# Kernel tuning notes

Measured on AMD Instinct MI355X. Metric: run time of the kernel, lower is better.

## Reference

```python
import jax, jax.numpy as jnp
import numpy as np

N_NODES = 50000
N_EDGES = 800000
F_IN = 512
NHID = 256
N_CLASSES = 10
N_GRAPHS = 64


def setup_inputs() -> dict:
    key = jax.random.key(0)
    ks = jax.random.split(key, 8)
    x = jax.random.normal(ks[0], (N_NODES, F_IN), dtype=jnp.float32)
    edge_index = jax.random.randint(ks[1], (2, N_EDGES), 0, N_NODES, dtype=jnp.int32)
    # sorted graph-assignment covering all N_GRAPHS segments (global max pool ids)
    batch = ((jnp.arange(N_NODES) * N_GRAPHS) // N_NODES).astype(jnp.int32)
    s1 = 1.0 / np.sqrt(F_IN)
    s2 = 1.0 / np.sqrt(NHID)
    W1 = jax.random.normal(ks[2], (F_IN, NHID), dtype=jnp.float32) * s1
    W2 = jax.random.normal(ks[3], (NHID, NHID), dtype=jnp.float32) * s2
    W3 = jax.random.normal(ks[4], (NHID, NHID), dtype=jnp.float32) * s2
    Wl = jax.random.normal(ks[5], (NHID, N_CLASSES), dtype=jnp.float32) * s2
    b1 = jnp.zeros((NHID,), jnp.float32)
    b2 = jnp.zeros((NHID,), jnp.float32)
    b3 = jnp.zeros((NHID,), jnp.float32)
    bl = jnp.zeros((N_CLASSES,), jnp.float32)
    return dict(x=x, edge_index=edge_index, batch=batch,
                W1=W1, b1=b1, W2=W2, b2=b2, W3=W3, b3=b3, Wl=Wl, bl=bl)


def reference(x, edge_index, batch, W1, b1, W2, b2, W3, b3, Wl, bl):
    n = x.shape[0]
    loop = jnp.arange(n, dtype=edge_index.dtype)
    src = jnp.concatenate([edge_index[0], loop])  # [E+N]
    dst = jnp.concatenate([edge_index[1], loop])
    # symmetric GCN normalization with self-loops: deg >= 1
    deg = jax.ops.segment_sum(jnp.ones_like(dst, jnp.float32), dst, num_segments=n)
    dinv = jax.lax.rsqrt(deg)
    norm = dinv[src] * dinv[dst]  # [E+N]

    def gcn(h, W, b):
        hw = h @ W                                   # [N, H] dense GEMM
        msg = hw[src] * norm[:, None]                # gather + scale [E+N, H]
        agg = jax.ops.segment_sum(msg, dst, num_segments=n)  # scatter-add
        return agg + b

    h = jax.nn.relu(gcn(x, W1, b1))
    h = jax.nn.relu(gcn(h, W2, b2))
    h = jax.nn.relu(gcn(h, W3, b3))
    g = jax.ops.segment_max(h, batch, num_segments=N_GRAPHS)  # global max pool [G, H]
    return jax.nn.log_softmax(g @ Wl + bl, axis=-1)
```

## Files before the change

kernel.cpp:

```cpp
#include <hip/hip_runtime.h>
#include <hip/hip_bf16.h>
#include <cstdint>
#include <cstddef>

typedef __attribute__((ext_vector_type(8))) short short8;
typedef __attribute__((ext_vector_type(4))) float f32x4;

__device__ __forceinline__ unsigned short f32_to_bf16_rn(float f) {
  unsigned int u = __float_as_uint(f);
  u += 0x7FFFu + ((u >> 16) & 1u);
  return (unsigned short)(u >> 16);
}
__device__ __forceinline__ float bf16_to_f32(unsigned short b) {
  return __uint_as_float(((unsigned int)b) << 16);
}
__device__ __forceinline__ void split_bf(float f, unsigned short& hi, unsigned short& lo) {
  hi = f32_to_bf16_rn(f);
  lo = f32_to_bf16_rn(f - bf16_to_f32(hi));
}
__device__ __forceinline__ float4 bf4_to_f4(ushort4 v) {
  float4 r;
  r.x = bf16_to_f32(v.x); r.y = bf16_to_f32(v.y);
  r.z = bf16_to_f32(v.z); r.w = bf16_to_f32(v.w);
  return r;
}

__device__ __forceinline__ void gload16(const void* g, const void* l) {
  __builtin_amdgcn_global_load_lds(
      (const __attribute__((address_space(1))) unsigned int*)g,
      (__attribute__((address_space(3))) unsigned int*)l, 16, 0, 0);
}

__global__ void k_init(int* cnt, int* cursor, float* g, int M, int GH) {
  int i = blockIdx.x * blockDim.x + threadIdx.x;
  int stride = gridDim.x * blockDim.x;
  for (int x = i; x < M; x += stride) { cnt[x] = 0; cursor[x] = 0; }
  for (int x = i; x < GH; x += stride) g[x] = 0.f;
}

__global__ void k_count(const int* __restrict__ dst, int* __restrict__ cnt, int E) {
  int i = blockIdx.x * blockDim.x + threadIdx.x;
  for (int e = i; e < E; e += gridDim.x * blockDim.x)
    atomicAdd(&cnt[dst[e]], 1);
}

__global__ void k_dinv(const int* __restrict__ cnt, float* __restrict__ dinv, int M) {
  int i = blockIdx.x * blockDim.x + threadIdx.x;
  if (i < M) dinv[i] = rsqrtf((float)(cnt[i] + 1));
}

__global__ void k_scan1(const int* __restrict__ cnt, int* __restrict__ excl,
                        int* __restrict__ bsum, int M) {
  __shared__ int s[256];
  int gid = blockIdx.x * 256 + threadIdx.x;
  int v = (gid < M) ? cnt[gid] : 0;
  s[threadIdx.x] = v;
  __syncthreads();
  for (int off = 1; off < 256; off <<= 1) {
    int t = (threadIdx.x >= off) ? s[threadIdx.x - off] : 0;
    __syncthreads();
    s[threadIdx.x] += t;
    __syncthreads();
  }
  if (gid < M) excl[gid] = s[threadIdx.x] - v;
  if (threadIdx.x == 255) bsum[blockIdx.x] = s[255];
}

__global__ void k_scan2(int* bsum, int nb) {
  __shared__ int s[256];
  int v = (threadIdx.x < nb) ? bsum[threadIdx.x] : 0;
  s[threadIdx.x] = v;
  __syncthreads();
  for (int off = 1; off < 256; off <<= 1) {
    int t = (threadIdx.x >= off) ? s[threadIdx.x - off] : 0;
    __syncthreads();
    s[threadIdx.x] += t;
    __syncthreads();
  }
  if (threadIdx.x < nb) bsum[threadIdx.x] = s[threadIdx.x] - v;
}

__global__ void k_scan3(int* row_ptr, const int* __restrict__ bsum, int M, int E) {
  int gid = blockIdx.x * 256 + threadIdx.x;
  if (gid < M) row_ptr[gid] += bsum[blockIdx.x];
  if (gid == 0) row_ptr[M] = E;
}

__global__ void k_scatter(const int* __restrict__ src, const int* __restrict__ dst,
                          const int* __restrict__ row_ptr, int* __restrict__ cursor,
                          int* __restrict__ eidx, int E) {
  int i = blockIdx.x * blockDim.x + threadIdx.x;
  for (int e = i; e < E; e += gridDim.x * blockDim.x) {
    int d = dst[e];
    int pos = atomicAdd(&cursor[d], 1);
    eidx[row_ptr[d] + pos] = src[e];
  }
}

__global__ void k_wtrans(const float* __restrict__ W, unsigned short* __restrict__ WTh,
                         unsigned short* __restrict__ WTl, int K) {
  int idx = blockIdx.x * 256 + threadIdx.x;
  if (idx >= K * 256) return;
  int n = idx / K, k = idx % K;
  float v = W[(size_t)k * 256 + n];
  unsigned short h, l;
  split_bf(v, h, l);
  WTh[(size_t)n * K + k] = h;
  WTl[(size_t)n * K + k] = l;
}

#define BM 64
#define BN 256
#define BK 32

template <bool AF32>
__global__ __launch_bounds__(256) void k_gemm(
    const float* __restrict__ Af,
    const unsigned short* __restrict__ Ahg, const unsigned short* __restrict__ Alg,
    const unsigned short* __restrict__ WTh, const unsigned short* __restrict__ WTl,
    const float* __restrict__ dinv, unsigned short* __restrict__ out, int M, int K) {
  constexpr int AHB = AF32 ? 8192 : 0;
  constexpr int ALB = AHB + 4096;
  constexpr int BHB = AF32 ? 16384 : 8192;
  constexpr int BLB = BHB + 16384;
  constexpr int LDSZ = BLB + 16384;
  __shared__ __align__(16) char lds[LDSZ];

  const int tid = threadIdx.x;
  const int lane = tid & 63;
  const int wv = tid >> 6;
  const int row0 = blockIdx.x * BM;
  const int ASTEP = AF32 ? BK * 4 : BK * 2;

  const char* gsrc[10];
  unsigned ldsoff[10];
#pragma unroll
  for (int i = 0; i < 10; ++i) {
    int c = wv + 4 * i;
    if (i < 2) {
      ldsoff[i] = (unsigned)(c * 1024);
      if constexpr (AF32) {
        int r = c * 8 + (lane >> 3);
        int sslot = (lane & 7) ^ (r & 7);
        int gr = row0 + r; gr = gr < M ? gr : (M - 1);
        gsrc[i] = (const char*)(Af + (size_t)gr * K + sslot * 4);
      } else {
        int plane = c >> 2;
        int r = (c & 3) * 16 + (lane >> 2);
        int sslot = (lane & 3) ^ ((r >> 1) & 3);
        int gr = row0 + r; gr = gr < M ? gr : (M - 1);
        const unsigned short* base = plane ? Alg : Ahg;
        gsrc[i] = (const char*)(base + (size_t)gr * K + sslot * 8);
      }
    } else {
      int cb = c - 8;
      ldsoff[i] = (unsigned)(BHB + cb * 1024);
      int plane = cb >> 4;
      int col = (cb & 15) * 16 + (lane >> 2);
      int sslot = (lane & 3) ^ ((col >> 1) & 3);
      const unsigned short* base = plane ? WTl : WTh;
      gsrc[i] = (const char*)(base + (size_t)col * K + sslot * 8);
    }
  }

  f32x4 acc[4][4] = {};
  const int fr = lane & 15;
  const int ks = lane >> 4;

  for (int k0 = 0; k0 < K; k0 += BK) {
#pragma unroll
    for (int i = 0; i < 10; ++i) {
      gload16(gsrc[i], lds + ldsoff[i]);
      gsrc[i] += (i < 2) ? ASTEP : (BK * 2);
    }
    __syncthreads();

    if constexpr (AF32) {
      int r = tid >> 2, q = tid & 3, rx = r & 7;
      float4 f0 = *(const float4*)&lds[(size_t)r * 128 + (((2 * q) ^ rx) * 16)];
      float4 f1 = *(const float4*)&lds[(size_t)r * 128 + (((2 * q + 1) ^ rx) * 16)];
      float f[8] = {f0.x, f0.y, f0.z, f0.w, f1.x, f1.y, f1.z, f1.w};
      short8 hv, lv;
#pragma unroll
      for (int j = 0; j < 8; ++j) {
        unsigned short h, l;
        split_bf(f[j], h, l);
        hv[j] = (short)h; lv[j] = (short)l;
      }
      int so = (q ^ ((r >> 1) & 3)) * 16;
      *(short8*)&lds[AHB + r * 64 + so] = hv;
      *(short8*)&lds[ALB + r * 64 + so] = lv;
      __syncthreads();
    }

    short8 ah[4], al[4];
#pragma unroll
    for (int m = 0; m < 4; ++m) {
      int rr = m * 16 + fr;
      int so = (ks ^ ((rr >> 1) & 3)) * 16;
      ah[m] = *(const short8*)&lds[AHB + rr * 64 + so];
      al[m] = *(const short8*)&lds[ALB + rr * 64 + so];
    }
#pragma unroll
    for (int n = 0; n < 4; ++n) {
      int cc = wv * 64 + n * 16 + fr;
      int so = (ks ^ ((cc >> 1) & 3)) * 16;
      short8 bh = *(const short8*)&lds[BHB + cc * 64 + so];
      short8 bl = *(const short8*)&lds[BLB + cc * 64 + so];
#pragma unroll
      for (int m = 0; m < 4; ++m) {
        acc[m][n] = __builtin_amdgcn_mfma_f32_16x16x32_bf16(ah[m], bh, acc[m][n], 0, 0, 0);
        acc[m][n] = __builtin_amdgcn_mfma_f32_16x16x32_bf16(ah[m], bl, acc[m][n], 0, 0, 0);
        acc[m][n] = __builtin_amdgcn_mfma_f32_16x16x32_bf16(al[m], bh, acc[m][n], 0, 0, 0);
      }
    }
    __syncthreads();
  }

  const int rq = (lane >> 4) * 4;
#pragma unroll
  for (int m = 0; m < 4; ++m) {
#pragma unroll
    for (int r = 0; r < 4; ++r) {
      int gr = row0 + m * 16 + rq + r;
      if (gr < M) {
        float s = dinv[gr];
#pragma unroll
        for (int n = 0; n < 4; ++n)
          out[(size_t)gr * BN + wv * 64 + n * 16 + fr] = f32_to_bf16_rn(acc[m][n][r] * s);
      }
    }
  }
}

__global__ __launch_bounds__(64) void k_aggregate(
    const unsigned short* __restrict__ hws, const int* __restrict__ eidx,
    const int* __restrict__ row_ptr, const float* __restrict__ dinv,
    const float* __restrict__ bias, unsigned short* __restrict__ out_hi,
    unsigned short* __restrict__ out_lo, float* __restrict__ out_f32, int M) {
  int i = blockIdx.x;
  if (i >= M) return;
  int t = threadIdx.x;
  float4 acc = bf4_to_f4(*(const ushort4*)(hws + (size_t)i * 256 + t * 4));
  int beg = row_ptr[i], end = row_ptr[i + 1];
  int e = beg;
  for (; e + 4 <= end; e += 4) {
    int s0 = eidx[e + 0], s1 = eidx[e + 1], s2 = eidx[e + 2], s3 = eidx[e + 3];
    ushort4 v0 = *(const ushort4*)(hws + (size_t)s0 * 256 + t * 4);
    ushort4 v1 = *(const ushort4*)(hws + (size_t)s1 * 256 + t * 4);
    ushort4 v2 = *(const ushort4*)(hws + (size_t)s2 * 256 + t * 4);
    ushort4 v3 = *(const ushort4*)(hws + (size_t)s3 * 256 + t * 4);
    float4 f0 = bf4_to_f4(v0), f1 = bf4_to_f4(v1);
    float4 f2 = bf4_to_f4(v2), f3 = bf4_to_f4(v3);
    acc.x += (f0.x + f1.x) + (f2.x + f3.x);
    acc.y += (f0.y + f1.y) + (f2.y + f3.y);
    acc.z += (f0.z + f1.z) + (f2.z + f3.z);
    acc.w += (f0.w + f1.w) + (f2.w + f3.w);
  }
  for (; e < end; ++e) {
    int s = eidx[e];
    float4 v = bf4_to_f4(*(const ushort4*)(hws + (size_t)s * 256 + t * 4));
    acc.x += v.x; acc.y += v.y; acc.z += v.z; acc.w += v.w;
  }
  float d = dinv[i];
  float4 b = *(const float4*)(bias + t * 4);
  float r[4];
  r[0] = fmaxf(fmaf(acc.x, d, b.x), 0.f);
  r[1] = fmaxf(fmaf(acc.y, d, b.y), 0.f);
  r[2] = fmaxf(fmaf(acc.z, d, b.z), 0.f);
  r[3] = fmaxf(fmaf(acc.w, d, b.w), 0.f);
  if (out_f32) {
    float4 o; o.x = r[0]; o.y = r[1]; o.z = r[2]; o.w = r[3];
    *(float4*)(out_f32 + (size_t)i * 256 + t * 4) = o;
  } else {
    ushort4 hv, lv;
    unsigned short h, l;
    split_bf(r[0], h, l); hv.x = h; lv.x = l;
    split_bf(r[1], h, l); hv.y = h; lv.y = l;
    split_bf(r[2], h, l); hv.z = h; lv.z = l;
    split_bf(r[3], h, l); hv.w = h; lv.w = l;
    *(ushort4*)(out_hi + (size_t)i * 256 + t * 4) = hv;
    *(ushort4*)(out_lo + (size_t)i * 256 + t * 4) = lv;
  }
}

__global__ __launch_bounds__(256) void k_pool(const float* __restrict__ h,
                                              const int* __restrict__ batch,
                                              float* __restrict__ g, int M) {
  int node0 = blockIdx.x * 32;
  if (node0 >= M) return;
  int t = threadIdx.x;
  int nEnd = min(node0 + 32, M);
  int cur = batch[node0];
  float acc = 0.f;
  for (int n = node0; n < nEnd; ++n) {
    int b = batch[n];
    if (b != cur) {
      atomicMax((int*)&g[(size_t)cur * 256 + t], __float_as_int(acc));
      acc = 0.f; cur = b;
    }
    acc = fmaxf(acc, h[(size_t)n * 256 + t]);
  }
  atomicMax((int*)&g[(size_t)cur * 256 + t], __float_as_int(acc));
}

__global__ __launch_bounds__(256) void k_classify(const float* __restrict__ g,
                                                  const float* __restrict__ Wl,
                                                  const float* __restrict__ bl,
                                                  float* __restrict__ out) {
  __shared__ float sg[256];
  __shared__ float logits[10];
  int b = blockIdx.x;
  sg[threadIdx.x] = g[(size_t)b * 256 + threadIdx.x];
  __syncthreads();
  if (threadIdx.x < 10) {
    float s = bl[threadIdx.x];
    for (int k = 0; k < 256; ++k) s = fmaf(sg[k], Wl[k * 10 + threadIdx.x], s);
    logits[threadIdx.x] = s;
  }
  __syncthreads();
  if (threadIdx.x == 0) {
    float m = logits[0];
    for (int c = 1; c < 10; c++) m = fmaxf(m, logits[c]);
    float sum = 0.f;
    for (int c = 0; c < 10; c++) sum += expf(logits[c] - m);
    float lse = m + logf(sum);
    for (int c = 0; c < 10; c++) out[b * 10 + c] = logits[c] - lse;
  }
}

static inline size_t align256(size_t x) { return (x + 255) & ~(size_t)255; }

extern "C" void kernel_launch(void* const* d_in, const int* in_sizes, int n_in,
                              void* d_out, int out_size, void* d_ws, size_t ws_size,
                              hipStream_t stream) {
  const float* x   = (const float*)d_in[0];
  const int*   ei  = (const int*)d_in[1];
  const int*   bat = (const int*)d_in[2];
  const float* W1  = (const float*)d_in[3];
  const float* b1  = (const float*)d_in[4];
  const float* W2  = (const float*)d_in[5];
  const float* b2  = (const float*)d_in[6];
  const float* W3  = (const float*)d_in[7];
  const float* b3  = (const float*)d_in[8];
  const float* Wl  = (const float*)d_in[9];
  const float* bl  = (const float*)d_in[10];
  float* out = (float*)d_out;

  const int M = in_sizes[0] / 512;
  const int E = in_sizes[1] / 2;
  const int G = out_size / 10;
  const int K1 = 512, H = 256;

  const int* src = ei;
  const int* dst = ei + E;

  char* p = (char*)d_ws;
  size_t off = 0;
  float* p_dinv = (float*)(p + off); off = align256(off + (size_t)M * 4);
  int* cnt      = (int*)(p + off);   off = align256(off + (size_t)M * 4);
  int* cursor   = (int*)(p + off);   off = align256(off + (size_t)M * 4);
  int* row_ptr  = (int*)(p + off);   off = align256(off + ((size_t)M + 1) * 4);
  int* bsum     = (int*)(p + off);   off = align256(off + 256 * 4);
  int* eidx     = (int*)(p + off);   off = align256(off + (size_t)E * 4);
  float* g      = (float*)(p + off); off = align256(off + (size_t)G * H * 4);
  unsigned short* WT1h = (unsigned short*)(p + off); off = align256(off + (size_t)H * K1 * 2);
  unsigned short* WT1l = (unsigned short*)(p + off); off = align256(off + (size_t)H * K1 * 2);
  unsigned short* WT2h = (unsigned short*)(p + off); off = align256(off + (size_t)H * H * 2);
  unsigned short* WT2l = (unsigned short*)(p + off); off = align256(off + (size_t)H * H * 2);
  unsigned short* WT3h = (unsigned short*)(p + off); off = align256(off + (size_t)H * H * 2);
  unsigned short* WT3l = (unsigned short*)(p + off); off = align256(off + (size_t)H * H * 2);
  unsigned short* hws = (unsigned short*)(p + off); off = align256(off + (size_t)M * H * 2);
  unsigned short* h_hi = (unsigned short*)(p + off); off += (size_t)M * H * 2;
  unsigned short* h_lo = (unsigned short*)(p + off); off = align256(off + (size_t)M * H * 2);
  float* bufC = (float*)h_hi;
  (void)ws_size;

  int nb = (M + 255) / 256;

  k_init<<<256, 256, 0, stream>>>(cnt, cursor, g, M, G * H);
  k_count<<<1024, 256, 0, stream>>>(dst, cnt, E);
  k_dinv<<<nb, 256, 0, stream>>>(cnt, p_dinv, M);
  k_scan1<<<nb, 256, 0, stream>>>(cnt, row_ptr, bsum, M);
  k_scan2<<<1, 256, 0, stream>>>(bsum, nb);
  k_scan3<<<nb, 256, 0, stream>>>(row_ptr, bsum, M, E);
  k_scatter<<<1024, 256, 0, stream>>>(src, dst, row_ptr, cursor, eidx, E);

  k_wtrans<<<(H * K1 + 255) / 256, 256, 0, stream>>>(W1, WT1h, WT1l, K1);
  k_wtrans<<<(H * H + 255) / 256, 256, 0, stream>>>(W2, WT2h, WT2l, H);
  k_wtrans<<<(H * H + 255) / 256, 256, 0, stream>>>(W3, WT3h, WT3l, H);

  int gblk = (M + BM - 1) / BM;
  k_gemm<true><<<gblk, 256, 0, stream>>>(x, nullptr, nullptr, WT1h, WT1l, p_dinv, hws, M, K1);
  k_aggregate<<<M, 64, 0, stream>>>(hws, eidx, row_ptr, p_dinv, b1, h_hi, h_lo, nullptr, M);
  k_gemm<false><<<gblk, 256, 0, stream>>>(nullptr, h_hi, h_lo, WT2h, WT2l, p_dinv, hws, M, H);
  k_aggregate<<<M, 64, 0, stream>>>(hws, eidx, row_ptr, p_dinv, b2, h_hi, h_lo, nullptr, M);
  k_gemm<false><<<gblk, 256, 0, stream>>>(nullptr, h_hi, h_lo, WT3h, WT3l, p_dinv, hws, M, H);
  k_aggregate<<<M, 64, 0, stream>>>(hws, eidx, row_ptr, p_dinv, b3, nullptr, nullptr, bufC, M);

  k_pool<<<(M + 31) / 32, 256, 0, stream>>>(bufC, bat, g, M);
  k_classify<<<G, 256, 0, stream>>>(g, Wl, bl, out);
}
```

Measured before the change: 598.5 us.

## Double-buffer GEMM LDS tiles and precast x to bf16 for layer one

Restructures the GEMM kernel into a two-stage LDS double buffer with async global-to-LDS prefetch of the next K tile, explicit vmcnt waits and raw barriers, so loads overlap MFMA work. The first-layer GEMM no longer converts fp32 x to split hi/lo bf16 inside the loop. A separate cast kernel writes a bf16 hi-only copy of x, and layer one drops the A-low MFMA term. This reduces in-loop conversion, memory traffic and MFMA count, but adds a full pass over x and lowers layer-one precision to one bf16 term for x.

Result: no change. 602.1 us (+0.6%).

```diff
diff --git a/kernel.cpp b/kernel.cpp
--- a/kernel.cpp
+++ b/kernel.cpp
@@ -97,6 +97,19 @@
   }
 }
 
+__global__ __launch_bounds__(256) void k_xcast(const float* __restrict__ x,
+                                               unsigned short* __restrict__ xh, int n4) {
+  int i = blockIdx.x * 256 + threadIdx.x;
+  int stride = gridDim.x * 256;
+  for (; i < n4; i += stride) {
+    float4 v = ((const float4*)x)[i];
+    ushort4 h;
+    h.x = f32_to_bf16_rn(v.x); h.y = f32_to_bf16_rn(v.y);
+    h.z = f32_to_bf16_rn(v.z); h.w = f32_to_bf16_rn(v.w);
+    ((ushort4*)xh)[i] = h;
+  }
+}
+
 __global__ void k_wtrans(const float* __restrict__ W, unsigned short* __restrict__ WTh,
                          unsigned short* __restrict__ WTl, int K) {
   int idx = blockIdx.x * 256 + threadIdx.x;
@@ -113,48 +126,38 @@
 #define BN 256
 #define BK 32
 
-template <bool AF32>
+template <bool ALO>
 __global__ __launch_bounds__(256) void k_gemm(
-    const float* __restrict__ Af,
     const unsigned short* __restrict__ Ahg, const unsigned short* __restrict__ Alg,
     const unsigned short* __restrict__ WTh, const unsigned short* __restrict__ WTl,
     const float* __restrict__ dinv, unsigned short* __restrict__ out, int M, int K) {
-  constexpr int AHB = AF32 ? 8192 : 0;
-  constexpr int ALB = AHB + 4096;
-  constexpr int BHB = AF32 ? 16384 : 8192;
-  constexpr int BLB = BHB + 16384;
-  constexpr int LDSZ = BLB + 16384;
-  __shared__ __align__(16) char lds[LDSZ];
+  constexpr int NACH = ALO ? 8 : 4;
+  constexpr int NCH = NACH + 32;
+  constexpr int NLD = NCH / 4;
+  constexpr int ABYT = NACH * 1024;
+  constexpr int BUFB = ABYT + 32768;
+  __shared__ __align__(16) char lds[2 * BUFB];
 
   const int tid = threadIdx.x;
   const int lane = tid & 63;
   const int wv = tid >> 6;
   const int row0 = blockIdx.x * BM;
-  const int ASTEP = AF32 ? BK * 4 : BK * 2;
-
-  const char* gsrc[10];
-  unsigned ldsoff[10];
-#pragma unroll
-  for (int i = 0; i < 10; ++i) {
+
+  const char* gsrc[NLD];
+  unsigned ldsoff[NLD];
+#pragma unroll
+  for (int i = 0; i < NLD; ++i) {
     int c = wv + 4 * i;
-    if (i < 2) {
-      ldsoff[i] = (unsigned)(c * 1024);
-      if constexpr (AF32) {
-        int r = c * 8 + (lane >> 3);
-        int sslot = (lane & 7) ^ (r & 7);
-        int gr = row0 + r; gr = gr < M ? gr : (M - 1);
-        gsrc[i] = (const char*)(Af + (size_t)gr * K + sslot * 4);
-      } else {
-        int plane = c >> 2;
-        int r = (c & 3) * 16 + (lane >> 2);
-        int sslot = (lane & 3) ^ ((r >> 1) & 3);
-        int gr = row0 + r; gr = gr < M ? gr : (M - 1);
-        const unsigned short* base = plane ? Alg : Ahg;
-        gsrc[i] = (const char*)(base + (size_t)gr * K + sslot * 8);
-      }
+    ldsoff[i] = (unsigned)(c * 1024);
+    if (c < NACH) {
+      int plane = ALO ? (c >> 2) : 0;
+      int r = (c & 3) * 16 + (lane >> 2);
+      int sslot = (lane & 3) ^ ((r >> 1) & 3);
+      int gr = row0 + r; gr = gr < M ? gr : (M - 1);
+      const unsigned short* base = plane ? Alg : Ahg;
+      gsrc[i] = (const char*)(base + (size_t)gr * K + sslot * 8);
     } else {
-      int cb = c - 8;
-      ldsoff[i] = (unsigned)(BHB + cb * 1024);
+      int cb = c - NACH;
       int plane = cb >> 4;
       int col = (cb & 15) * 16 + (lane >> 2);
       int sslot = (lane & 3) ^ ((col >> 1) & 3);
@@ -166,55 +169,52 @@
   f32x4 acc[4][4] = {};
   const int fr = lane & 15;
   const int ks = lane >> 4;
-
-  for (int k0 = 0; k0 < K; k0 += BK) {
-#pragma unroll
-    for (int i = 0; i < 10; ++i) {
-      gload16(gsrc[i], lds + ldsoff[i]);
-      gsrc[i] += (i < 2) ? ASTEP : (BK * 2);
-    }
-    __syncthreads();
-
-    if constexpr (AF32) {
-      int r = tid >> 2, q = tid & 3, rx = r & 7;
-      float4 f0 = *(const float4*)&lds[(size_t)r * 128 + (((2 * q) ^ rx) * 16)];
-      float4 f1 = *(const float4*)&lds[(size_t)r * 128 + (((2 * q + 1) ^ rx) * 16)];
-      float f[8] = {f0.x, f0.y, f0.z, f0.w, f1.x, f1.y, f1.z, f1.w};
-      short8 hv, lv;
-#pragma unroll
-      for (int j = 0; j < 8; ++j) {
-        unsigned short h, l;
-        split_bf(f[j], h, l);
-        hv[j] = (short)h; lv[j] = (short)l;
-      }
-      int so = (q ^ ((r >> 1) & 3)) * 16;
-      *(short8*)&lds[AHB + r * 64 + so] = hv;
-      *(short8*)&lds[ALB + r * 64 + so] = lv;
-      __syncthreads();
-    }
+  const int NT = K / BK;
+
+#pragma unroll
+  for (int i = 0; i < NLD; ++i) { gload16(gsrc[i], lds + ldsoff[i]); gsrc[i] += 64; }
+
+  auto phase = [&](int curo, int nxto, bool dostage) {
+    if (dostage) {
+#pragma unroll
+      for (int i = 0; i < NLD; ++i) { gload16(gsrc[i], lds + nxto + ldsoff[i]); gsrc[i] += 64; }
+      if constexpr (ALO) asm volatile("s_waitcnt vmcnt(10)" ::: "memory");
+      else               asm volatile("s_waitcnt vmcnt(9)" ::: "memory");
+    } else {
+      asm volatile("s_waitcnt vmcnt(0)" ::: "memory");
+    }
+    __builtin_amdgcn_s_barrier();
+    __builtin_amdgcn_sched_barrier(0);
 
     short8 ah[4], al[4];
 #pragma unroll
     for (int m = 0; m < 4; ++m) {
       int rr = m * 16 + fr;
       int so = (ks ^ ((rr >> 1) & 3)) * 16;
-      ah[m] = *(const short8*)&lds[AHB + rr * 64 + so];
-      al[m] = *(const short8*)&lds[ALB + rr * 64 + so];
+      ah[m] = *(const short8*)&lds[curo + rr * 64 + so];
+      if constexpr (ALO) al[m] = *(const short8*)&lds[curo + 4096 + rr * 64 + so];
     }
 #pragma unroll
     for (int n = 0; n < 4; ++n) {
       int cc = wv * 64 + n * 16 + fr;
       int so = (ks ^ ((cc >> 1) & 3)) * 16;
-      short8 bh = *(const short8*)&lds[BHB + cc * 64 + so];
-      short8 bl = *(const short8*)&lds[BLB + cc * 64 + so];
+      short8 bh = *(const short8*)&lds[curo + ABYT + cc * 64 + so];
+      short8 bl = *(const short8*)&lds[curo + ABYT + 16384 + cc * 64 + so];
 #pragma unroll
       for (int m = 0; m < 4; ++m) {
         acc[m][n] = __builtin_amdgcn_mfma_f32_16x16x32_bf16(ah[m], bh, acc[m][n], 0, 0, 0);
         acc[m][n] = __builtin_amdgcn_mfma_f32_16x16x32_bf16(ah[m], bl, acc[m][n], 0, 0, 0);
-        acc[m][n] = __builtin_amdgcn_mfma_f32_16x16x32_bf16(al[m], bh, acc[m][n], 0, 0, 0);
+        if constexpr (ALO)
+          acc[m][n] = __builtin_amdgcn_mfma_f32_16x16x32_bf16(al[m], bh, acc[m][n], 0, 0, 0);
       }
     }
-    __syncthreads();
+    __builtin_amdgcn_sched_barrier(0);
+    __builtin_amdgcn_s_barrier();
+  };
+
+  for (int t = 0; t < NT; t += 2) {
+    phase(0, BUFB, true);
+    phase(BUFB, 0, t + 2 < NT);
   }
 
   const int rq = (lane >> 4) * 4;
@@ -373,6 +373,7 @@
   unsigned short* hws = (unsigned short*)(p + off); off = align256(off + (size_t)M * H * 2);
   unsigned short* h_hi = (unsigned short*)(p + off); off += (size_t)M * H * 2;
   unsigned short* h_lo = (unsigned short*)(p + off); off = align256(off + (size_t)M * H * 2);
+  unsigned short* xh = h_lo;
   float* bufC = (float*)h_hi;
   (void)ws_size;
 
@@ -386,16 +387,17 @@
   k_scan3<<<nb, 256, 0, stream>>>(row_ptr, bsum, M, E);
   k_scatter<<<1024, 256, 0, stream>>>(src, dst, row_ptr, cursor, eidx, E);
 
+  k_xcast<<<2048, 256, 0, stream>>>(x, xh, M * K1 / 4);
   k_wtrans<<<(H * K1 + 255) / 256, 256, 0, stream>>>(W1, WT1h, WT1l, K1);
   k_wtrans<<<(H * H + 255) / 256, 256, 0, stream>>>(W2, WT2h, WT2l, H);
   k_wtrans<<<(H * H + 255) / 256, 256, 0, stream>>>(W3, WT3h, WT3l, H);
 
   int gblk = (M + BM - 1) / BM;
-  k_gemm<true><<<gblk, 256, 0, stream>>>(x, nullptr, nullptr, WT1h, WT1l, p_dinv, hws, M, K1);
+  k_gemm<false><<<gblk, 256, 0, stream>>>(xh, nullptr, WT1h, WT1l, p_dinv, hws, M, K1);
   k_aggregate<<<M, 64, 0, stream>>>(hws, eidx, row_ptr, p_dinv, b1, h_hi, h_lo, nullptr, M);
-  k_gemm<false><<<gblk, 256, 0, stream>>>(nullptr, h_hi, h_lo, WT2h, WT2l, p_dinv, hws, M, H);
+  k_gemm<true><<<gblk, 256, 0, stream>>>(h_hi, h_lo, WT2h, WT2l, p_dinv, hws, M, H);
   k_aggregate<<<M, 64, 0, stream>>>(hws, eidx, row_ptr, p_dinv, b2, h_hi, h_lo, nullptr, M);
-  k_gemm<false><<<gblk, 256, 0, stream>>>(nullptr, h_hi, h_lo, WT3h, WT3l, p_dinv, hws, M, H);
+  k_gemm<true><<<gblk, 256, 0, stream>>>(h_hi, h_lo, WT3h, WT3l, p_dinv, hws, M, H);
   k_aggregate<<<M, 64, 0, stream>>>(hws, eidx, row_ptr, p_dinv, b3, nullptr, nullptr, bufC, M);
 
   k_pool<<<(M + 31) / 32, 256, 0, stream>>>(bufC, bat, g, M);
```
